# Kernel optimization log

Hardware: AMD Instinct MI355X
Metric: run time of the kernel (lower is better)

## Reference

```python
import jax, jax.numpy as jnp
import numpy as np

B, T, C, H, N = 2, 2048, 2048, 32, 64
EPS_GN = 1e-5 * 8 ** 2  # eps * head_size_divisor^2


def _bf16(t):
    # kernel inputs are cast to bfloat16 in the original module
    return t.astype(jnp.bfloat16).astype(jnp.float32)


def _rwkv7_scan(r, k, v, w, a, b, s0):
    """Generalized delta-rule recurrence (fused_recurrent_rwkv7 semantics).
    r,k,v,w,a,b: [B,T,H,N]; s0: [B,H,N,N] with layout [key, value].
    S_t = diag(exp(w_t)) S + b_t (a_t^T S) + k_t v_t^T ; o_t = r_t^T S_t."""
    def step(S, ts):
        rt, kt, vt, wt, at, bt = ts  # each [B,H,N]
        sa = jnp.einsum('bhk,bhkv->bhv', at, S)
        S = S * jnp.exp(wt)[..., None] + bt[..., None] * sa[..., None, :] + kt[..., None] * vt[..., None, :]
        o = jnp.einsum('bhk,bhkv->bhv', rt, S)
        return S, o
    mv = lambda t: jnp.moveaxis(t, 1, 0)  # [B,T,H,N] -> [T,B,H,N]
    S, o = jax.lax.scan(step, s0, (mv(r), mv(k), mv(v), mv(w), mv(a), mv(b)))
    return jnp.moveaxis(o, 0, 1), S


def _forward(x, shift_state, wkv_state, v_first, x_r, x_w, x_k, x_v, x_a, x_g,
             w0, w1, w2, a0, a1, a2, v0, v1, v2, g1, g2, k_k, k_a, r_k,
             W_r, W_k, W_v, W_o, ln_w, ln_b):
    xx = jnp.concatenate([shift_state[:, None, :], x[:, :-1]], axis=1) - x
    xr, xw, xk, xv, xa, xg = (x + xx * m for m in (x_r, x_w, x_k, x_v, x_a, x_g))
    r = xr @ W_r
    w = -jax.nn.softplus(-(w0 + jnp.tanh(xw @ w1) @ w2)) - 0.5
    k = xk @ W_k
    v = xv @ W_v
    v = v + (v_first - v) * jax.nn.sigmoid(v0 + (xv @ v1) @ v2)  # layer_id > 0 branch
    a = jax.nn.sigmoid(a0 + (xa @ a1) @ a2)
    g = jax.nn.sigmoid(xg @ g1) @ g2
    kk = (k * k_k).reshape(B, T, H, N)
    kk = kk / jnp.maximum(jnp.linalg.norm(kk, axis=-1, keepdims=True), 1e-12)
    kk = kk.reshape(B, T, C)
    k = k * (1.0 + (a - 1.0) * k_a)
    hd = lambda t: _bf16(t).reshape(B, T, H, N)
    o, S = _rwkv7_scan(hd(r), hd(k), hd(v), hd(w), hd(-kk), hd(kk * a), wkv_state)
    y = o.reshape(B, T, H, N)
    # GroupNorm with H groups over C channels
    mu = y.mean(-1, keepdims=True)
    var = ((y - mu) ** 2).mean(-1, keepdims=True)
    y = ((y - mu) / jnp.sqrt(var + EPS_GN)).reshape(B, T, C) * ln_w + ln_b
    rr, k4, vv = r.reshape(B, T, H, N), k.reshape(B, T, H, N), v.reshape(B, T, H, N)
    y = y + ((rr * k4 * r_k).sum(-1, keepdims=True) * vv).reshape(B, T, C)
    out = (y * g) @ W_o
    return out, x[:, -1], S


def setup_inputs() -> dict:
    key = jax.random.key(0)
    ks = iter(jax.random.split(key, 40))
    rn = lambda shape, s=0.02: jax.random.normal(next(ks), shape, jnp.float32) * s
    ru = lambda shape: jax.random.uniform(next(ks), shape, jnp.float32)
    return dict(
        x=rn((B, T, C), 1.0), shift_state=rn((B, C), 1.0),
        wkv_state=jnp.zeros((B, H, N, N), jnp.float32), v_first=rn((B, T, C), 1.0),
        x_r=ru((1, 1, C)), x_w=ru((1, 1, C)), x_k=ru((1, 1, C)),
        x_v=ru((1, 1, C)), x_a=ru((1, 1, C)), x_g=ru((1, 1, C)),
        w0=rn((1, 1, C), 0.5) - 4.0, w1=rn((C, 64)), w2=rn((64, C)),
        a0=jnp.zeros((1, 1, C), jnp.float32), a1=rn((C, 64)), a2=rn((64, C)),
        v0=jnp.ones((1, 1, C), jnp.float32), v1=rn((C, 32)), v2=rn((32, C)),
        g1=rn((C, 128)), g2=rn((128, C)),
        k_k=jnp.full((1, 1, C), 0.85, jnp.float32), k_a=jnp.ones((1, 1, C), jnp.float32),
        r_k=rn((H, N), 0.1),
        W_r=rn((C, C), C ** -0.5), W_k=rn((C, C), C ** -0.5),
        W_v=rn((C, C), C ** -0.5), W_o=rn((C, C), C ** -0.5),
        ln_w=jnp.ones((C,), jnp.float32), ln_b=jnp.zeros((C,), jnp.float32))


def reference(x, shift_state, wkv_state, v_first, x_r, x_w, x_k, x_v, x_a, x_g,
              w0, w1, w2, a0, a1, a2, v0, v1, v2, g1, g2, k_k, k_a, r_k,
              W_r, W_k, W_v, W_o, ln_w, ln_b):
    return _forward(x, shift_state, wkv_state, v_first, x_r, x_w, x_k, x_v, x_a, x_g,
                    w0, w1, w2, a0, a1, a2, v0, v1, v2, g1, g2, k_k, k_a, r_k,
                    W_r, W_k, W_v, W_o, ln_w, ln_b)
```

## Files before the change

### kernel.cpp

```cpp
#include <hip/hip_runtime.h>
#include <cstdint>
#include <cmath>

#define B_ 2
#define T_ 2048
#define C_ 2048
#define H_ 32
#define BT_ (B_ * T_)
#define BTC_ ((size_t)B_ * T_ * C_)
#define L_ 128
#define NC_ 16

typedef __attribute__((ext_vector_type(4))) float f32x4;
typedef __attribute__((ext_vector_type(2))) float f32x2;
typedef __attribute__((ext_vector_type(8))) short bf16x8;
typedef __attribute__((ext_vector_type(4))) unsigned short us4;
typedef __attribute__((ext_vector_type(4))) int i32x4;

__device__ __forceinline__ unsigned short f2bf(float f) {
  union { float f; unsigned int u; } c; c.f = f;
  unsigned int u = c.u;
  return (unsigned short)((u + 0x7FFFu + ((u >> 16) & 1u)) >> 16);
}
__device__ __forceinline__ float bf2f(unsigned short h) {
  union { unsigned int u; float f; } c; c.u = ((unsigned int)h) << 16;
  return c.f;
}
__device__ __forceinline__ float rlane(float v, int lane) {
  return __int_as_float(__builtin_amdgcn_readlane(__float_as_int(v), lane));
}
__device__ __forceinline__ void split4(f32x4 v, us4& h, us4& l) {
  h.x = f2bf(v.x); l.x = f2bf(v.x - bf2f(h.x));
  h.y = f2bf(v.y); l.y = f2bf(v.y - bf2f(h.y));
  h.z = f2bf(v.z); l.z = f2bf(v.z - bf2f(h.z));
  h.w = f2bf(v.w); l.w = f2bf(v.w - bf2f(h.w));
}
__device__ __forceinline__ void g2l(const void* g, void* l) {
  __builtin_amdgcn_global_load_lds((const __attribute__((address_space(1))) void*)g,
                                   (__attribute__((address_space(3))) void*)l, 16, 0, 0);
}

__global__ __launch_bounds__(256) void k_mix(
    const float* __restrict__ x, const float* __restrict__ shift,
    const float* __restrict__ m_r, const float* __restrict__ m_w,
    const float* __restrict__ m_k, const float* __restrict__ m_v,
    const float* __restrict__ m_a, const float* __restrict__ m_g,
    unsigned short* __restrict__ r_h, unsigned short* __restrict__ r_l,
    unsigned short* __restrict__ k_h, unsigned short* __restrict__ k_l,
    unsigned short* __restrict__ v_h, unsigned short* __restrict__ v_l,
    unsigned short* __restrict__ o_w, unsigned short* __restrict__ o_a,
    unsigned short* __restrict__ o_g,
    float* __restrict__ xlast) {
  size_t i4 = ((size_t)blockIdx.x * 256 + threadIdx.x) * 4;
  int c = (int)(i4 % C_);
  size_t bt = i4 / C_;
  int t = (int)(bt % T_);
  int b = (int)(bt / T_);
  f32x4 xv = *(const f32x4*)(x + i4);
  f32x4 pv = (t == 0) ? *(const f32x4*)(shift + (size_t)b * C_ + c)
                      : *(const f32x4*)(x + i4 - C_);
  f32x4 dx = pv - xv;
#define MIXHL(mp, oh, ol) { f32x4 mm = *(const f32x4*)(mp + c); f32x4 rr = xv + dx * mm; \
    us4 hh, ll; split4(rr, hh, ll); *(us4*)(oh + i4) = hh; *(us4*)(ol + i4) = ll; }
#define MIXH(mp, oh) { f32x4 mm = *(const f32x4*)(mp + c); f32x4 rr = xv + dx * mm; \
    us4 pk; pk.x = f2bf(rr.x); pk.y = f2bf(rr.y); pk.z = f2bf(rr.z); pk.w = f2bf(rr.w); \
    *(us4*)(oh + i4) = pk; }
  MIXHL(m_r, r_h, r_l) MIXHL(m_k, k_h, k_l) MIXHL(m_v, v_h, v_l)
  MIXH(m_w, o_w) MIXH(m_a, o_a) MIXH(m_g, o_g)
#undef MIXHL
#undef MIXH
  if (t == T_ - 1) *(f32x4*)(xlast + (size_t)b * C_ + c) = xv;
}

__global__ __launch_bounds__(256) void k_tr(const float* __restrict__ in,
                                            unsigned short* __restrict__ out,
                                            int R, int Cc) {
  __shared__ float tile[32][33];
  int c0 = blockIdx.x * 32, r0 = blockIdx.y * 32;
  int tid = threadIdx.x;
  int rr = tid >> 3, c4 = (tid & 7) * 4;
  f32x4 v = *(const f32x4*)(in + (size_t)(r0 + rr) * Cc + c0 + c4);
  tile[rr][c4] = v.x; tile[rr][c4 + 1] = v.y; tile[rr][c4 + 2] = v.z; tile[rr][c4 + 3] = v.w;
  __syncthreads();
  int cc = tid >> 3, r4 = (tid & 7) * 4;
  us4 o;
  o.x = f2bf(tile[r4][cc]); o.y = f2bf(tile[r4 + 1][cc]);
  o.z = f2bf(tile[r4 + 2][cc]); o.w = f2bf(tile[r4 + 3][cc]);
  *(us4*)(out + (size_t)(c0 + cc) * R + r0 + r4) = o;
}

__global__ __launch_bounds__(256) void k_trs(const float* __restrict__ in,
                                             unsigned short* __restrict__ oh,
                                             unsigned short* __restrict__ ol,
                                             int R, int Cc) {
  __shared__ float tile[32][33];
  int c0 = blockIdx.x * 32, r0 = blockIdx.y * 32;
  int tid = threadIdx.x;
  int rr = tid >> 3, c4 = (tid & 7) * 4;
  f32x4 v = *(const f32x4*)(in + (size_t)(r0 + rr) * Cc + c0 + c4);
  tile[rr][c4] = v.x; tile[rr][c4 + 1] = v.y; tile[rr][c4 + 2] = v.z; tile[rr][c4 + 3] = v.w;
  __syncthreads();
  int cc = tid >> 3, r4 = (tid & 7) * 4;
  f32x4 w = { tile[r4][cc], tile[r4 + 1][cc], tile[r4 + 2][cc], tile[r4 + 3][cc] };
  us4 h, l; split4(w, h, l);
  size_t o = (size_t)(c0 + cc) * R + r0 + r4;
  *(us4*)(oh + o) = h; *(us4*)(ol + o) = l;
}

__global__ __launch_bounds__(256) void k_gemm(
    const unsigned short* __restrict__ X, const unsigned short* __restrict__ Wt,
    void* __restrict__ out, int M, int N, int K, int mode) {
  __shared__ alignas(16) unsigned short As[128 * 32];
  __shared__ alignas(16) unsigned short Bs[128 * 32];
  const int tid = threadIdx.x;
  const int lane = tid & 63, wave = tid >> 6;
  const int wr = wave >> 1, wc = wave & 1;
  const int lm = lane & 15, lq = lane >> 4;
  const int m0 = blockIdx.y * 128, n0 = blockIdx.x * 128;
  const int srow = (lane >> 2);
  const int kcol = (lane & 3) * 8;
  f32x4 acc[4][4];
#pragma unroll
  for (int i = 0; i < 4; ++i)
#pragma unroll
    for (int j = 0; j < 4; ++j) acc[i][j] = (f32x4){0.f, 0.f, 0.f, 0.f};

  for (int k0 = 0; k0 < K; k0 += 32) {
#pragma unroll
    for (int p = 0; p < 2; ++p) {
      int row = wave * 32 + p * 16 + srow;
      g2l(X + (size_t)(m0 + row) * K + k0 + kcol, As + (wave * 2 + p) * 512);
      int n = n0 + row; if (n > N - 1) n = N - 1;
      g2l(Wt + (size_t)n * K + k0 + kcol, Bs + (wave * 2 + p) * 512);
    }
    __syncthreads();
    bf16x8 af[4], bfr[4];
#pragma unroll
    for (int i = 0; i < 4; ++i)
      af[i] = *(const bf16x8*)(As + (size_t)(wr * 64 + i * 16 + lm) * 32 + lq * 8);
#pragma unroll
    for (int j = 0; j < 4; ++j)
      bfr[j] = *(const bf16x8*)(Bs + (size_t)(wc * 64 + j * 16 + lm) * 32 + lq * 8);
#pragma unroll
    for (int i = 0; i < 4; ++i)
#pragma unroll
      for (int j = 0; j < 4; ++j)
        acc[i][j] = __builtin_amdgcn_mfma_f32_16x16x32_bf16(af[i], bfr[j], acc[i][j], 0, 0, 0);
    __syncthreads();
  }
#pragma unroll
  for (int i = 0; i < 4; ++i)
#pragma unroll
    for (int j = 0; j < 4; ++j) {
      int n = n0 + wc * 64 + j * 16 + lm;
      if (n >= N) continue;
      int mb = m0 + wr * 64 + i * 16 + lq * 4;
#pragma unroll
      for (int r = 0; r < 4; ++r) {
        float val = acc[i][j][r];
        size_t off = (size_t)(mb + r) * N + n;
        if (mode == 0) {
          ((float*)out)[off] = val;
        } else {
          if (mode == 2) val = tanhf(val);
          else if (mode == 3) val = 1.0f / (1.0f + __expf(-val));
          ((unsigned short*)out)[off] = f2bf(val);
        }
      }
    }
}

__global__ __launch_bounds__(256) void k_gemm2(
    const unsigned short* __restrict__ Xh, const unsigned short* __restrict__ Xl, int xlo,
    const unsigned short* __restrict__ Wh, const unsigned short* __restrict__ Wl, int wlo,
    void* __restrict__ out, int M, int N, int K, int mode) {
  __shared__ alignas(16) unsigned short Ah[128 * 32];
  __shared__ alignas(16) unsigned short Al[128 * 32];
  __shared__ alignas(16) unsigned short Bh[128 * 32];
  __shared__ alignas(16) unsigned short Bl[128 * 32];
  const int tid = threadIdx.x;
  const int lane = tid & 63, wave = tid >> 6;
  const int wr = wave >> 1, wc = wave & 1;
  const int lm = lane & 15, lq = lane >> 4;
  const int m0 = blockIdx.y * 128, n0 = blockIdx.x * 128;
  const int srow = (lane >> 2);
  const int kcol = (lane & 3) * 8;
  f32x4 acc[4][4];
#pragma unroll
  for (int i = 0; i < 4; ++i)
#pragma unroll
    for (int j = 0; j < 4; ++j) acc[i][j] = (f32x4){0.f, 0.f, 0.f, 0.f};

  for (int k0 = 0; k0 < K; k0 += 32) {
#pragma unroll
    for (int p = 0; p < 2; ++p) {
      int row = wave * 32 + p * 16 + srow;
      int off = (wave * 2 + p) * 512;
      size_t ga = (size_t)(m0 + row) * K + k0 + kcol;
      g2l(Xh + ga, Ah + off);
      if (xlo) g2l(Xl + ga, Al + off);
      int n = n0 + row; if (n > N - 1) n = N - 1;
      size_t gb = (size_t)n * K + k0 + kcol;
      g2l(Wh + gb, Bh + off);
      if (wlo) g2l(Wl + gb, Bl + off);
    }
    __syncthreads();
    bf16x8 ah[4], bh[4];
#pragma unroll
    for (int i = 0; i < 4; ++i)
      ah[i] = *(const bf16x8*)(Ah + (size_t)(wr * 64 + i * 16 + lm) * 32 + lq * 8);
#pragma unroll
    for (int j = 0; j < 4; ++j)
      bh[j] = *(const bf16x8*)(Bh + (size_t)(wc * 64 + j * 16 + lm) * 32 + lq * 8);
#pragma unroll
    for (int i = 0; i < 4; ++i)
#pragma unroll
      for (int j = 0; j < 4; ++j)
        acc[i][j] = __builtin_amdgcn_mfma_f32_16x16x32_bf16(ah[i], bh[j], acc[i][j], 0, 0, 0);
    if (xlo) {
      bf16x8 al[4];
#pragma unroll
      for (int i = 0; i < 4; ++i)
        al[i] = *(const bf16x8*)(Al + (size_t)(wr * 64 + i * 16 + lm) * 32 + lq * 8);
#pragma unroll
      for (int i = 0; i < 4; ++i)
#pragma unroll
        for (int j = 0; j < 4; ++j)
          acc[i][j] = __builtin_amdgcn_mfma_f32_16x16x32_bf16(al[i], bh[j], acc[i][j], 0, 0, 0);
    }
    if (wlo) {
      bf16x8 bl[4];
#pragma unroll
      for (int j = 0; j < 4; ++j)
        bl[j] = *(const bf16x8*)(Bl + (size_t)(wc * 64 + j * 16 + lm) * 32 + lq * 8);
#pragma unroll
      for (int i = 0; i < 4; ++i)
#pragma unroll
        for (int j = 0; j < 4; ++j)
          acc[i][j] = __builtin_amdgcn_mfma_f32_16x16x32_bf16(ah[i], bl[j], acc[i][j], 0, 0, 0);
    }
    __syncthreads();
  }
#pragma unroll
  for (int i = 0; i < 4; ++i)
#pragma unroll
    for (int j = 0; j < 4; ++j) {
      int n = n0 + wc * 64 + j * 16 + lm;
      if (n >= N) continue;
      int mb = m0 + wr * 64 + i * 16 + lq * 4;
#pragma unroll
      for (int r = 0; r < 4; ++r) {
        float val = acc[i][j][r];
        size_t off = (size_t)(mb + r) * N + n;
        if (mode == 0) {
          ((float*)out)[off] = val;
        } else {
          if (mode == 2) val = tanhf(val);
          else if (mode == 3) val = 1.0f / (1.0f + __expf(-val));
          ((unsigned short*)out)[off] = f2bf(val);
        }
      }
    }
}

__global__ __launch_bounds__(256) void k_pre(
    const float* __restrict__ rp, const float* __restrict__ kp, float* __restrict__ vp,
    const unsigned short* __restrict__ ww, const unsigned short* __restrict__ aa,
    const unsigned short* __restrict__ vv,
    const float* __restrict__ vfirst,
    const float* __restrict__ w0, const float* __restrict__ a0, const float* __restrict__ v0,
    const float* __restrict__ kkc, const float* __restrict__ kac,
    const float* __restrict__ rkw,
    unsigned short* __restrict__ rb, unsigned short* __restrict__ wb,
    unsigned short* __restrict__ kb, unsigned short* __restrict__ vb,
    unsigned short* __restrict__ ab, unsigned short* __restrict__ bb,
    float* __restrict__ dp) {
  int gw = blockIdx.x * 4 + (threadIdx.x >> 6);
  int l = threadIdx.x & 63;
  int h = gw & (H_ - 1);
  size_t bt = (size_t)(gw >> 5);
  size_t idx = bt * C_ + h * 64 + l;
  int c = h * 64 + l;
  float rf = rp[idx], kf = kp[idx], vr = vp[idx];
  float z = -(w0[c] + bf2f(ww[idx]));
  float sp = (z > 15.f) ? z : log1pf(__expf(z));
  float wv = -sp - 0.5f;
  float ag = 1.f / (1.f + __expf(-(a0[c] + bf2f(aa[idx]))));
  float sv = 1.f / (1.f + __expf(-(v0[c] + bf2f(vv[idx]))));
  float vf = vr + (vfirst[idx] - vr) * sv;
  float kkv = kf * kkc[c];
  float ss = kkv * kkv;
#pragma unroll
  for (int m = 1; m < 64; m <<= 1) ss += __shfl_xor(ss, m);
  float nrm = fmaxf(sqrtf(ss), 1e-12f);
  float kkn = kkv / nrm;
  float ks = kf * (1.f + (ag - 1.f) * kac[c]);
  vp[idx] = vf;
  float bon = rf * ks * rkw[c];
#pragma unroll
  for (int m = 1; m < 64; m <<= 1) bon += __shfl_xor(bon, m);
  if (l == 0) dp[bt * H_ + h] = bon;
  rb[idx] = f2bf(rf); wb[idx] = f2bf(wv); kb[idx] = f2bf(ks);
  vb[idx] = f2bf(vf); ab[idx] = f2bf(-kkn); bb[idx] = f2bf(kkn * ag);
}

__global__ __launch_bounds__(256) void k_scanP(
    const unsigned short* __restrict__ wb, const unsigned short* __restrict__ kb,
    const unsigned short* __restrict__ vb, const unsigned short* __restrict__ ab,
    const unsigned short* __restrict__ bb,
    float* __restrict__ Pg, float* __restrict__ Ug) {
  const int blk = blockIdx.x;
  const int c = blk & (NC_ - 1), bh = blk >> 4;
  const int b = bh >> 5, h = bh & (H_ - 1);
  const int l = threadIdx.x & 63;
  const int kg = __builtin_amdgcn_readfirstlane(threadIdx.x >> 6);
  const int kg16 = kg * 16;
  __shared__ f32x2 part[2][256];
  size_t base = (size_t)b * ((size_t)T_ * C_) + (size_t)(c * L_) * C_ + h * 64 + l;
  float P[16], U[16];
#pragma unroll
  for (int i = 0; i < 16; ++i) { P[i] = (kg16 + i == l) ? 1.f : 0.f; U[i] = 0.f; }
  float pw[4], pk[4], pv[4], pa[4], pb[4];
#pragma unroll
  for (int s = 0; s < 4; ++s) {
    size_t a_ = base + (size_t)s * C_;
    pw[s] = bf2f(wb[a_]); pk[s] = bf2f(kb[a_]); pv[s] = bf2f(vb[a_]);
    pa[s] = bf2f(ab[a_]); pb[s] = bf2f(bb[a_]);
  }
  float saP = pa[0];
  float saU = 0.f;
  for (int t0 = 0; t0 < L_; t0 += 4) {
#pragma unroll
    for (int u = 0; u < 4; ++u) {
      const int t = t0 + u;
      float wl = pw[u], kl = pk[u], vl = pv[u], bl = pb[u];
      float an = pa[(u + 1) & 3];
      if (t + 4 < L_) {
        size_t a_ = base + (size_t)(t + 4) * C_;
        pw[u] = bf2f(wb[a_]); pk[u] = bf2f(kb[a_]); pv[u] = bf2f(vb[a_]);
        pa[u] = bf2f(ab[a_]); pb[u] = bf2f(bb[a_]);
      }
      float ew = exp2f(wl * 1.4426950408889634f);
      float psP = 0.f, psU = 0.f;
#pragma unroll
      for (int i = 0; i < 16; ++i) {
        int ki = kg16 + i;
        float ewk = rlane(ew, ki), bk = rlane(bl, ki), kk = rlane(kl, ki);
        P[i] = fmaf(P[i], ewk, bk * saP);
        U[i] = fmaf(U[i], ewk, fmaf(bk, saU, kk * vl));
        float ak = rlane(an, ki);
        psP = fmaf(ak, P[i], psP);
        psU = fmaf(ak, U[i], psU);
      }
      part[t & 1][kg * 64 + l] = (f32x2){psP, psU};
      __syncthreads();
      f32x2 q0 = part[t & 1][l], q1 = part[t & 1][64 + l],
            q2 = part[t & 1][128 + l], q3 = part[t & 1][192 + l];
      saP = (q0.x + q1.x) + (q2.x + q3.x);
      saU = (q0.y + q1.y) + (q2.y + q3.y);
    }
  }
  size_t pb_ = (size_t)blk * 4096;
#pragma unroll
  for (int i = 0; i < 16; ++i) {
    Pg[pb_ + (size_t)l * 64 + kg16 + i] = P[i];
    Ug[pb_ + (size_t)(kg16 + i) * 64 + l] = U[i];
  }
}

__global__ __launch_bounds__(256) void k_scanC(
    const float* __restrict__ Pg, const float* __restrict__ Ug,
    const float* __restrict__ s0, float* __restrict__ Scg, float* __restrict__ sout) {
  const int bh = blockIdx.x;
  const int l = threadIdx.x & 63;
  const int kg = __builtin_amdgcn_readfirstlane(threadIdx.x >> 6);
  const int kg16 = kg * 16;
  const int tid = threadIdx.x;
  __shared__ float Sb[4096];
#pragma unroll
  for (int q = 0; q < 4; ++q) {
    int e = tid * 16 + q * 4;
    *(f32x4*)(Sb + e) = *(const f32x4*)(s0 + (size_t)bh * 4096 + e);
  }
  __syncthreads();
  for (int c = 0; c < NC_; ++c) {
    size_t cb = ((size_t)bh * NC_ + c) * 4096;
#pragma unroll
    for (int q = 0; q < 4; ++q) {
      int e = tid * 16 + q * 4;
      *(f32x4*)(Scg + cb + e) = *(const f32x4*)(Sb + e);
    }
    const float* Pt = Pg + cb;
    const float* Uc = Ug + cb;
    float acc[16];
#pragma unroll
    for (int i = 0; i < 16; ++i) acc[i] = Uc[(size_t)(kg16 + i) * 64 + l];
    for (int j = 0; j < 64; ++j) {
      float s = Sb[j * 64 + l];
#pragma unroll
      for (int i = 0; i < 16; ++i) acc[i] = fmaf(Pt[j * 64 + kg16 + i], s, acc[i]);
    }
    __syncthreads();
#pragma unroll
    for (int i = 0; i < 16; ++i) Sb[(kg16 + i) * 64 + l] = acc[i];
    __syncthreads();
  }
#pragma unroll
  for (int q = 0; q < 4; ++q) {
    int e = tid * 16 + q * 4;
    *(f32x4*)(sout + (size_t)bh * 4096 + e) = *(const f32x4*)(Sb + e);
  }
}

__global__ __launch_bounds__(256) void k_scanR(
    const unsigned short* __restrict__ rb, const unsigned short* __restrict__ wb,
    const unsigned short* __restrict__ kb, const unsigned short* __restrict__ vb,
    const unsigned short* __restrict__ ab, const unsigned short* __restrict__ bb,
    const float* __restrict__ Scg, float* __restrict__ o) {
  const int blk = blockIdx.x;
  const int c = blk & (NC_ - 1), bh = blk >> 4;
  const int b = bh >> 5, h = bh & (H_ - 1);
  const int l = threadIdx.x & 63;
  const int kg = __builtin_amdgcn_readfirstlane(threadIdx.x >> 6);
  const int kg16 = kg * 16;
  __shared__ f32x2 part[2][256];
  size_t base = (size_t)b * ((size_t)T_ * C_) + (size_t)(c * L_) * C_ + h * 64 + l;
  float S[16];
  size_t cb = (size_t)blk * 4096;
#pragma unroll
  for (int i = 0; i < 16; ++i) S[i] = Scg[cb + (size_t)(kg16 + i) * 64 + l];
  float pr[4], pw[4], pk[4], pv[4], pa[4], pb[4];
#pragma unroll
  for (int s = 0; s < 4; ++s) {
    size_t a_ = base + (size_t)s * C_;
    pr[s] = bf2f(rb[a_]); pw[s] = bf2f(wb[a_]); pk[s] = bf2f(kb[a_]);
    pv[s] = bf2f(vb[a_]); pa[s] = bf2f(ab[a_]); pb[s] = bf2f(bb[a_]);
  }
  {
    float ps = 0.f;
#pragma unroll
    for (int i = 0; i < 16; ++i) ps = fmaf(rlane(pa[0], kg16 + i), S[i], ps);
    part[0][kg * 64 + l] = (f32x2){0.f, ps};
  }
  __syncthreads();
  float sa = part[0][l].y + part[0][64 + l].y + part[0][128 + l].y + part[0][192 + l].y;
  for (int t0 = 0; t0 < L_; t0 += 4) {
#pragma unroll
    for (int u = 0; u < 4; ++u) {
      const int t = t0 + u;
      float rl = pr[u], wl = pw[u], kl = pk[u], vl = pv[u], bl = pb[u];
      float an = pa[(u + 1) & 3];
      if (t + 4 < L_) {
        size_t a_ = base + (size_t)(t + 4) * C_;
        pr[u] = bf2f(rb[a_]); pw[u] = bf2f(wb[a_]); pk[u] = bf2f(kb[a_]);
        pv[u] = bf2f(vb[a_]); pa[u] = bf2f(ab[a_]); pb[u] = bf2f(bb[a_]);
      }
      float ew = exp2f(wl * 1.4426950408889634f);
      float po = 0.f, ps = 0.f;
#pragma unroll
      for (int i = 0; i < 16; ++i) {
        int ki = kg16 + i;
        float ewk = rlane(ew, ki), bk = rlane(bl, ki), kk = rlane(kl, ki);
        S[i] = fmaf(S[i], ewk, fmaf(bk, sa, kk * vl));
        po = fmaf(rlane(rl, ki), S[i], po);
        ps = fmaf(rlane(an, ki), S[i], ps);
      }
      part[(t + 1) & 1][kg * 64 + l] = (f32x2){po, ps};
      __syncthreads();
      f32x2 q0 = part[(t + 1) & 1][l], q1 = part[(t + 1) & 1][64 + l],
            q2 = part[(t + 1) & 1][128 + l], q3 = part[(t + 1) & 1][192 + l];
      if (kg == 0) o[base + (size_t)t * C_] = (q0.x + q1.x) + (q2.x + q3.x);
      sa = (q0.y + q1.y) + (q2.y + q3.y);
    }
  }
}

__global__ __launch_bounds__(256) void k_post(
    const float* __restrict__ o, const float* __restrict__ vp, const float* __restrict__ gp,
    const float* __restrict__ dp,
    const float* __restrict__ lnw, const float* __restrict__ lnb,
    unsigned short* __restrict__ z) {
  int gw = blockIdx.x * 4 + (threadIdx.x >> 6);
  int l = threadIdx.x & 63;
  int h = gw & (H_ - 1);
  size_t bt = (size_t)(gw >> 5);
  size_t idx = bt * C_ + h * 64 + l;
  int c = h * 64 + l;
  float ov = o[idx];
  float s1 = ov;
#pragma unroll
  for (int m = 1; m < 64; m <<= 1) s1 += __shfl_xor(s1, m);
  float mu = s1 * (1.f / 64.f);
  float d = ov - mu;
  float s2 = d * d;
#pragma unroll
  for (int m = 1; m < 64; m <<= 1) s2 += __shfl_xor(s2, m);
  float var = s2 * (1.f / 64.f);
  float y = d * rsqrtf(var + 6.4e-4f);
  y = y * lnw[c] + lnb[c];
  y = fmaf(dp[bt * H_ + h], vp[idx], y);
  z[idx] = f2bf(y * gp[idx]);
}

extern "C" void kernel_launch(void* const* d_in, const int* in_sizes, int n_in,
                              void* d_out, int out_size, void* d_ws, size_t ws_size,
                              hipStream_t stream) {
  const float* x      = (const float*)d_in[0];
  const float* shift  = (const float*)d_in[1];
  const float* wkv    = (const float*)d_in[2];
  const float* vfirst = (const float*)d_in[3];
  const float* x_r    = (const float*)d_in[4];
  const float* x_w    = (const float*)d_in[5];
  const float* x_k    = (const float*)d_in[6];
  const float* x_v    = (const float*)d_in[7];
  const float* x_a    = (const float*)d_in[8];
  const float* x_g    = (const float*)d_in[9];
  const float* w0     = (const float*)d_in[10];
  const float* w1     = (const float*)d_in[11];
  const float* w2     = (const float*)d_in[12];
  const float* a0     = (const float*)d_in[13];
  const float* a1     = (const float*)d_in[14];
  const float* a2     = (const float*)d_in[15];
  const float* v0     = (const float*)d_in[16];
  const float* v1     = (const float*)d_in[17];
  const float* v2     = (const float*)d_in[18];
  const float* g1     = (const float*)d_in[19];
  const float* g2     = (const float*)d_in[20];
  const float* k_k    = (const float*)d_in[21];
  const float* k_a    = (const float*)d_in[22];
  const float* r_k    = (const float*)d_in[23];
  const float* W_r    = (const float*)d_in[24];
  const float* W_k    = (const float*)d_in[25];
  const float* W_v    = (const float*)d_in[26];
  const float* W_o    = (const float*)d_in[27];
  const float* ln_w   = (const float*)d_in[28];
  const float* ln_b   = (const float*)d_in[29];

  char* wp = (char*)d_ws;
  auto alloc = [&](size_t bytes) { char* p = wp; wp += (bytes + 255) & ~(size_t)255; return p; };
  const size_t SB = BTC_ * 2;
  const size_t SF = BTC_ * 4;

  unsigned short* w1t = (unsigned short*)alloc((size_t)C_ * 64 * 2);
  unsigned short* w2t = (unsigned short*)alloc((size_t)C_ * 64 * 2);
  unsigned short* a1t = (unsigned short*)alloc((size_t)C_ * 64 * 2);
  unsigned short* a2t = (unsigned short*)alloc((size_t)C_ * 64 * 2);
  unsigned short* v1t = (unsigned short*)alloc((size_t)C_ * 32 * 2);
  unsigned short* v2t = (unsigned short*)alloc((size_t)C_ * 32 * 2);
  unsigned short* g1t = (unsigned short*)alloc((size_t)C_ * 128 * 2);
  unsigned short* g2t = (unsigned short*)alloc((size_t)C_ * 128 * 2);
  unsigned short* hw  = (unsigned short*)alloc((size_t)BT_ * 64 * 2);
  unsigned short* ha  = (unsigned short*)alloc((size_t)BT_ * 64 * 2);
  unsigned short* hv  = (unsigned short*)alloc((size_t)BT_ * 32 * 2);
  unsigned short* hg  = (unsigned short*)alloc((size_t)BT_ * 128 * 2);
  unsigned short* Wt2 = (unsigned short*)alloc((size_t)C_ * C_ * 2 * 2);
  float* dp           = (float*)alloc((size_t)BT_ * H_ * 4);
  unsigned short* xw  = (unsigned short*)alloc(SB);
  unsigned short* xa  = (unsigned short*)alloc(SB);
  unsigned short* xg  = (unsigned short*)alloc(SB);
  unsigned short* xr2 = (unsigned short*)alloc(2 * SB);
  unsigned short* xk2 = (unsigned short*)alloc(2 * SB);
  unsigned short* xv2 = (unsigned short*)alloc(2 * SB);
  float* rbuf         = (float*)alloc(SF);
  unsigned short* vbb = (unsigned short*)alloc(SB);

  unsigned short* Wh = Wt2;
  unsigned short* Wl = Wt2 + (size_t)C_ * C_;
  unsigned short* xr_h = xr2, *xr_l = xr2 + BTC_;
  unsigned short* xk_h = xk2, *xk_l = xk2 + BTC_;
  unsigned short* xv_h = xv2, *xv_l = xv2 + BTC_;
  float* kbuf = (float*)xr2;
  float* vbuf = (float*)xk2;
  unsigned short* rb = xv2;
  unsigned short* kb = xv2 + BTC_;
  float* gfull = rbuf;
  unsigned short* zbuf = (unsigned short*)xr2;
  float* Pg  = (float*)xr2;
  float* Ug  = Pg + (size_t)1024 * 4096;
  float* Scg = (float*)Wt2;

  float* outp  = (float*)d_out;
  float* xlast = outp + BTC_;
  float* soutp = outp + BTC_ + (size_t)B_ * C_;
  float* obuf  = outp;

  auto tr = [&](const float* in, unsigned short* out, int R, int Cc) {
    k_tr<<<dim3(Cc / 32, R / 32), 256, 0, stream>>>(in, out, R, Cc);
  };
  auto gemm = [&](const unsigned short* X, const unsigned short* Wtp, void* out,
                  int M, int N, int K, int mode) {
    k_gemm<<<dim3((N + 127) / 128, M / 128), 256, 0, stream>>>(X, Wtp, out, M, N, K, mode);
  };
  auto gemm2 = [&](const unsigned short* Xh_, const unsigned short* Xl_, int xlo,
                   const unsigned short* Wh_, const unsigned short* Wl_, int wlo,
                   void* out, int M, int N, int K, int mode) {
    k_gemm2<<<dim3((N + 127) / 128, M / 128), 256, 0, stream>>>(Xh_, Xl_, xlo, Wh_, Wl_, wlo,
                                                                out, M, N, K, mode);
  };

  k_mix<<<(int)(BTC_ / 4 / 256), 256, 0, stream>>>(x, shift, x_r, x_w, x_k, x_v, x_a, x_g,
                                                   xr_h, xr_l, xk_h, xk_l, xv_h, xv_l,
                                                   xw, xa, xg, xlast);
  tr(w1, w1t, C_, 64);  tr(w2, w2t, 64, C_);
  tr(a1, a1t, C_, 64);  tr(a2, a2t, 64, C_);
  tr(v1, v1t, C_, 32);  tr(v2, v2t, 32, C_);
  tr(g1, g1t, C_, 128); tr(g2, g2t, 128, C_);

  gemm(xw, w1t, hw, BT_, 64, C_, 2);
  gemm(xa, a1t, ha, BT_, 64, C_, 1);
  gemm2(xv_h, xv_l, 1, v1t, nullptr, 0, hv, BT_, 32, C_, 1);
  gemm(xg, g1t, hg, BT_, 128, C_, 3);

  k_trs<<<dim3(C_ / 32, C_ / 32), 256, 0, stream>>>(W_r, Wh, Wl, C_, C_);
  gemm2(xr_h, xr_l, 1, Wh, Wl, 1, rbuf, BT_, C_, C_, 0);
  k_trs<<<dim3(C_ / 32, C_ / 32), 256, 0, stream>>>(W_k, Wh, Wl, C_, C_);
  gemm2(xk_h, xk_l, 1, Wh, Wl, 1, kbuf, BT_, C_, C_, 0);
  k_trs<<<dim3(C_ / 32, C_ / 32), 256, 0, stream>>>(W_v, Wh, Wl, C_, C_);
  gemm2(xv_h, xv_l, 1, Wh, Wl, 1, vbuf, BT_, C_, C_, 0);

  gemm(hw, w2t, xw, BT_, C_, 64, 1);
  gemm(ha, a2t, xa, BT_, C_, 64, 1);
  gemm(hv, v2t, xg, BT_, C_, 32, 1);

  k_pre<<<BT_ * H_ / 4, 256, 0, stream>>>(rbuf, kbuf, vbuf, xw, xa, xg, vfirst,
                                          w0, a0, v0, k_k, k_a, r_k,
                                          rb, xw, kb, vbb, xa, xg, dp);

  gemm(hg, g2t, gfull, BT_, C_, 128, 0);

  k_scanP<<<B_ * H_ * NC_, 256, 0, stream>>>(xw, kb, vbb, xa, xg, Pg, Ug);
  k_scanC<<<B_ * H_, 256, 0, stream>>>(Pg, Ug, wkv, Scg, soutp);
  k_scanR<<<B_ * H_ * NC_, 256, 0, stream>>>(rb, xw, kb, vbb, xa, xg, Scg, obuf);

  k_post<<<BT_ * H_ / 4, 256, 0, stream>>>(obuf, vbuf, gfull, dp, ln_w, ln_b, zbuf);

  tr(W_o, Wh, C_, C_);
  gemm(zbuf, Wh, outp, BT_, C_, C_, 0);
}
```

Baseline: 1.626 ms.

## Fuse chunk output into scanP via r^T P projection; add GEMM block swizzle

New measurement: 1.466 ms. -9.8%, faster.

```diff
diff --git a/kernel.cpp b/kernel.cpp
--- a/kernel.cpp
+++ b/kernel.cpp
@@ -116,7 +116,11 @@
   const int lane = tid & 63, wave = tid >> 6;
   const int wr = wave >> 1, wc = wave & 1;
   const int lm = lane & 15, lq = lane >> 4;
-  const int m0 = blockIdx.y * 128, n0 = blockIdx.x * 128;
+  const int gx = gridDim.x;
+  const int nwg = gx * gridDim.y;
+  const int bid = blockIdx.y * gx + blockIdx.x;
+  const int sz = (bid & 7) * (nwg >> 3) + (bid >> 3);
+  const int m0 = (sz / gx) * 128, n0 = (sz % gx) * 128;
   const int srow = (lane >> 2);
   const int kcol = (lane & 3) * 8;
   f32x4 acc[4][4];
@@ -182,7 +186,11 @@
   const int lane = tid & 63, wave = tid >> 6;
   const int wr = wave >> 1, wc = wave & 1;
   const int lm = lane & 15, lq = lane >> 4;
-  const int m0 = blockIdx.y * 128, n0 = blockIdx.x * 128;
+  const int gx = gridDim.x;
+  const int nwg = gx * gridDim.y;
+  const int bid = blockIdx.y * gx + blockIdx.x;
+  const int sz = (bid & 7) * (nwg >> 3) + (bid >> 3);
+  const int m0 = (sz / gx) * 128, n0 = (sz % gx) * 128;
   const int srow = (lane >> 2);
   const int kcol = (lane & 3) * 8;
   f32x4 acc[4][4];
@@ -305,25 +313,29 @@
 }
 
 __global__ __launch_bounds__(256) void k_scanP(
+    const unsigned short* __restrict__ rb,
     const unsigned short* __restrict__ wb, const unsigned short* __restrict__ kb,
     const unsigned short* __restrict__ vb, const unsigned short* __restrict__ ab,
     const unsigned short* __restrict__ bb,
-    float* __restrict__ Pg, float* __restrict__ Ug) {
+    float* __restrict__ Pg, float* __restrict__ Ug,
+    unsigned short* __restrict__ Zg, float* __restrict__ o) {
   const int blk = blockIdx.x;
   const int c = blk & (NC_ - 1), bh = blk >> 4;
   const int b = bh >> 5, h = bh & (H_ - 1);
   const int l = threadIdx.x & 63;
   const int kg = __builtin_amdgcn_readfirstlane(threadIdx.x >> 6);
   const int kg16 = kg * 16;
-  __shared__ f32x2 part[2][256];
+  __shared__ f32x4 part[2][256];
   size_t base = (size_t)b * ((size_t)T_ * C_) + (size_t)(c * L_) * C_ + h * 64 + l;
+  size_t zbase = (size_t)blk * 8192;
   float P[16], U[16];
 #pragma unroll
   for (int i = 0; i < 16; ++i) { P[i] = (kg16 + i == l) ? 1.f : 0.f; U[i] = 0.f; }
-  float pw[4], pk[4], pv[4], pa[4], pb[4];
+  float pr[4], pw[4], pk[4], pv[4], pa[4], pb[4];
 #pragma unroll
   for (int s = 0; s < 4; ++s) {
     size_t a_ = base + (size_t)s * C_;
+    pr[s] = bf2f(rb[a_]);
     pw[s] = bf2f(wb[a_]); pk[s] = bf2f(kb[a_]); pv[s] = bf2f(vb[a_]);
     pa[s] = bf2f(ab[a_]); pb[s] = bf2f(bb[a_]);
   }
@@ -333,31 +345,39 @@
 #pragma unroll
     for (int u = 0; u < 4; ++u) {
       const int t = t0 + u;
-      float wl = pw[u], kl = pk[u], vl = pv[u], bl = pb[u];
+      float rl_ = pr[u], wl = pw[u], kl = pk[u], vl = pv[u], bl = pb[u];
       float an = pa[(u + 1) & 3];
       if (t + 4 < L_) {
         size_t a_ = base + (size_t)(t + 4) * C_;
+        pr[u] = bf2f(rb[a_]);
         pw[u] = bf2f(wb[a_]); pk[u] = bf2f(kb[a_]); pv[u] = bf2f(vb[a_]);
         pa[u] = bf2f(ab[a_]); pb[u] = bf2f(bb[a_]);
       }
       float ew = exp2f(wl * 1.4426950408889634f);
-      float psP = 0.f, psU = 0.f;
+      float psP = 0.f, psU = 0.f, zs = 0.f, ys = 0.f;
 #pragma unroll
       for (int i = 0; i < 16; ++i) {
         int ki = kg16 + i;
         float ewk = rlane(ew, ki), bk = rlane(bl, ki), kk = rlane(kl, ki);
         P[i] = fmaf(P[i], ewk, bk * saP);
         U[i] = fmaf(U[i], ewk, fmaf(bk, saU, kk * vl));
-        float ak = rlane(an, ki);
+        float ak = rlane(an, ki), rk = rlane(rl_, ki);
         psP = fmaf(ak, P[i], psP);
         psU = fmaf(ak, U[i], psU);
+        zs = fmaf(rk, P[i], zs);
+        ys = fmaf(rk, U[i], ys);
       }
-      part[t & 1][kg * 64 + l] = (f32x2){psP, psU};
+      part[t & 1][kg * 64 + l] = (f32x4){psP, psU, zs, ys};
       __syncthreads();
-      f32x2 q0 = part[t & 1][l], q1 = part[t & 1][64 + l],
+      f32x4 q0 = part[t & 1][l], q1 = part[t & 1][64 + l],
             q2 = part[t & 1][128 + l], q3 = part[t & 1][192 + l];
       saP = (q0.x + q1.x) + (q2.x + q3.x);
       saU = (q0.y + q1.y) + (q2.y + q3.y);
+      if (kg == 0) {
+        o[base + (size_t)t * C_] = (q0.w + q1.w) + (q2.w + q3.w);
+      } else if (kg == 1) {
+        Zg[zbase + t * 64 + l] = f2bf((q0.z + q1.z) + (q2.z + q3.z));
+      }
     }
   }
   size_t pb_ = (size_t)blk * 4096;
@@ -412,66 +432,32 @@
   }
 }
 
-__global__ __launch_bounds__(256) void k_scanR(
-    const unsigned short* __restrict__ rb, const unsigned short* __restrict__ wb,
-    const unsigned short* __restrict__ kb, const unsigned short* __restrict__ vb,
-    const unsigned short* __restrict__ ab, const unsigned short* __restrict__ bb,
-    const float* __restrict__ Scg, float* __restrict__ o) {
+__global__ __launch_bounds__(256) void k_scanO(
+    const unsigned short* __restrict__ Zg, const float* __restrict__ Scg,
+    float* __restrict__ o) {
   const int blk = blockIdx.x;
   const int c = blk & (NC_ - 1), bh = blk >> 4;
   const int b = bh >> 5, h = bh & (H_ - 1);
   const int l = threadIdx.x & 63;
-  const int kg = __builtin_amdgcn_readfirstlane(threadIdx.x >> 6);
-  const int kg16 = kg * 16;
-  __shared__ f32x2 part[2][256];
-  size_t base = (size_t)b * ((size_t)T_ * C_) + (size_t)(c * L_) * C_ + h * 64 + l;
-  float S[16];
-  size_t cb = (size_t)blk * 4096;
-#pragma unroll
-  for (int i = 0; i < 16; ++i) S[i] = Scg[cb + (size_t)(kg16 + i) * 64 + l];
-  float pr[4], pw[4], pk[4], pv[4], pa[4], pb[4];
-#pragma unroll
-  for (int s = 0; s < 4; ++s) {
-    size_t a_ = base + (size_t)s * C_;
-    pr[s] = bf2f(rb[a_]); pw[s] = bf2f(wb[a_]); pk[s] = bf2f(kb[a_]);
-    pv[s] = bf2f(vb[a_]); pa[s] = bf2f(ab[a_]); pb[s] = bf2f(bb[a_]);
-  }
-  {
-    float ps = 0.f;
-#pragma unroll
-    for (int i = 0; i < 16; ++i) ps = fmaf(rlane(pa[0], kg16 + i), S[i], ps);
-    part[0][kg * 64 + l] = (f32x2){0.f, ps};
-  }
-  __syncthreads();
-  float sa = part[0][l].y + part[0][64 + l].y + part[0][128 + l].y + part[0][192 + l].y;
-  for (int t0 = 0; t0 < L_; t0 += 4) {
-#pragma unroll
-    for (int u = 0; u < 4; ++u) {
-      const int t = t0 + u;
-      float rl = pr[u], wl = pw[u], kl = pk[u], vl = pv[u], bl = pb[u];
-      float an = pa[(u + 1) & 3];
-      if (t + 4 < L_) {
-        size_t a_ = base + (size_t)(t + 4) * C_;
-        pr[u] = bf2f(rb[a_]); pw[u] = bf2f(wb[a_]); pk[u] = bf2f(kb[a_]);
-        pv[u] = bf2f(vb[a_]); pa[u] = bf2f(ab[a_]); pb[u] = bf2f(bb[a_]);
-      }
-      float ew = exp2f(wl * 1.4426950408889634f);
-      float po = 0.f, ps = 0.f;
-#pragma unroll
-      for (int i = 0; i < 16; ++i) {
-        int ki = kg16 + i;
-        float ewk = rlane(ew, ki), bk = rlane(bl, ki), kk = rlane(kl, ki);
-        S[i] = fmaf(S[i], ewk, fmaf(bk, sa, kk * vl));
-        po = fmaf(rlane(rl, ki), S[i], po);
-        ps = fmaf(rlane(an, ki), S[i], ps);
-      }
-      part[(t + 1) & 1][kg * 64 + l] = (f32x2){po, ps};
-      __syncthreads();
-      f32x2 q0 = part[(t + 1) & 1][l], q1 = part[(t + 1) & 1][64 + l],
-            q2 = part[(t + 1) & 1][128 + l], q3 = part[(t + 1) & 1][192 + l];
-      if (kg == 0) o[base + (size_t)t * C_] = (q0.x + q1.x) + (q2.x + q3.x);
-      sa = (q0.y + q1.y) + (q2.y + q3.y);
-    }
+  const int w = threadIdx.x >> 6;
+  float S[64];
+  const float* Sp = Scg + (size_t)blk * 4096 + l;
+#pragma unroll
+  for (int k = 0; k < 64; ++k) S[k] = Sp[(size_t)k * 64];
+  size_t zb = (size_t)blk * 8192;
+  size_t ob = (size_t)b * ((size_t)T_ * C_) + (size_t)(c * L_) * C_ + h * 64 + l;
+  for (int tt = 0; tt < 32; ++tt) {
+    int t = w * 32 + tt;
+    float zv = bf2f(Zg[zb + t * 64 + l]);
+    float a0_ = 0.f, a1_ = 0.f, a2_ = 0.f, a3_ = 0.f;
+#pragma unroll
+    for (int k = 0; k < 64; k += 4) {
+      a0_ = fmaf(rlane(zv, k), S[k], a0_);
+      a1_ = fmaf(rlane(zv, k + 1), S[k + 1], a1_);
+      a2_ = fmaf(rlane(zv, k + 2), S[k + 2], a2_);
+      a3_ = fmaf(rlane(zv, k + 3), S[k + 3], a3_);
+    }
+    o[ob + (size_t)t * C_] += (a0_ + a1_) + (a2_ + a3_);
   }
 }
 
@@ -577,7 +563,8 @@
   unsigned short* zbuf = (unsigned short*)xr2;
   float* Pg  = (float*)xr2;
   float* Ug  = Pg + (size_t)1024 * 4096;
-  float* Scg = (float*)Wt2;
+  unsigned short* zg = Wt2;
+  float* Scg = (float*)xw;
 
   float* outp  = (float*)d_out;
   float* xlast = outp + BTC_;
@@ -628,9 +615,9 @@
 
   gemm(hg, g2t, gfull, BT_, C_, 128, 0);
 
-  k_scanP<<<B_ * H_ * NC_, 256, 0, stream>>>(xw, kb, vbb, xa, xg, Pg, Ug);
+  k_scanP<<<B_ * H_ * NC_, 256, 0, stream>>>(rb, xw, kb, vbb, xa, xg, Pg, Ug, zg, obuf);
   k_scanC<<<B_ * H_, 256, 0, stream>>>(Pg, Ug, wkv, Scg, soutp);
-  k_scanR<<<B_ * H_ * NC_, 256, 0, stream>>>(rb, xw, kb, vbb, xa, xg, Scg, obuf);
+  k_scanO<<<B_ * H_ * NC_, 256, 0, stream>>>(zg, Scg, obuf);
 
   k_post<<<BT_ * H_ / 4, 256, 0, stream>>>(obuf, vbuf, gfull, dp, ln_w, ln_b, zbuf);
 
```
